# Kernel optimization log

Measured on AMD Instinct MI355X. Metric: run time of the kernel, lower is better.

Reference implementation:

```python
import jax, jax.numpy as jnp
import numpy as np

V, E, H, R, RD = 32000, 300, 300, 50, 50  # vocab, word-emb, hidden, rel vocab, rel emb
B, N = 32, 128                            # trees per batch, nodes per tree


def setup_inputs() -> dict:
    key = jax.random.key(0)
    ks = jax.random.split(key, 10)
    root_hidden = jax.random.normal(ks[0], (B, H), jnp.float32)
    relations = jax.random.randint(ks[1], (B, N), 0, R, jnp.int32)
    prev_words = jax.random.randint(ks[2], (B, N), 0, V, jnp.int32)
    # topologically sorted parent pointers: parent[i] in [-1, i-1]; -1 = virtual root
    rng = np.random.default_rng(0)
    parents = np.full((B, N), -1, dtype=np.int32)
    for i in range(1, N):
        parents[:, i] = rng.integers(-1, i, size=B)
    parents = jnp.asarray(parents)
    s_in = 1.0 / np.float32(np.sqrt(RD + E))
    s_h = 1.0 / np.float32(np.sqrt(H))
    emb = jax.random.normal(ks[3], (V, E), jnp.float32) * 0.02
    rel_emb = jax.random.normal(ks[4], (R, RD), jnp.float32) * 0.02
    W_ih = jax.random.normal(ks[5], (4 * H, RD + E), jnp.float32) * s_in
    W_hh = jax.random.normal(ks[6], (4 * H, H), jnp.float32) * s_h
    b_ih = jnp.zeros((4 * H,), jnp.float32)
    b_hh = jnp.zeros((4 * H,), jnp.float32)
    W_out = jax.random.normal(ks[7], (V, H), jnp.float32) * s_h
    b_out = jnp.zeros((V,), jnp.float32)
    return {"root_hidden": root_hidden, "relations": relations, "prev_words": prev_words,
            "parents": parents, "emb": emb, "rel_emb": rel_emb, "W_ih": W_ih, "W_hh": W_hh,
            "b_ih": b_ih, "b_hh": b_hh, "W_out": W_out, "b_out": b_out}


def reference(root_hidden, relations, prev_words, parents, emb, rel_emb,
              W_ih, W_hh, b_ih, b_hh, W_out, b_out):
    # per-node input: rel embedding ++ (teacher-forced) previous word embedding
    x = jnp.concatenate([rel_emb[relations], emb[prev_words]], axis=-1)  # [B,N,RD+E]
    xg = jnp.einsum('bni,gi->bng', x, W_ih) + b_ih                       # [B,N,4H]

    def one_tree(h0, xg_t, pars):
        n = pars.shape[0]
        h_buf = jnp.zeros((n + 1, H), xg_t.dtype).at[0].set(h0)
        c_buf = jnp.zeros((n + 1, H), xg_t.dtype).at[0].set(h0)  # original: hidden=(h,h)

        def step(carry, inp):
            hb, cb = carry
            xg_i, par, idx = inp
            ph = hb[par + 1]
            pc = cb[par + 1]
            gates = xg_i + ph @ W_hh.T + b_hh
            i_g, f_g, g_g, o_g = jnp.split(gates, 4)
            c = jax.nn.sigmoid(f_g) * pc + jax.nn.sigmoid(i_g) * jnp.tanh(g_g)
            h = jax.nn.sigmoid(o_g) * jnp.tanh(c)
            return (hb.at[idx + 1].set(h), cb.at[idx + 1].set(c)), h

        _, hs = jax.lax.scan(step, (h_buf, c_buf), (xg_t, pars, jnp.arange(n)))
        return hs  # [N,H]

    hs = jax.vmap(one_tree)(root_hidden, xg, parents)          # [B,N,H]
    logits = jnp.einsum('bnh,vh->bnv', hs, W_out) + b_out      # [B,N,V]
    return logits
```

## Files before the change

kernel.cpp:

```cpp
#include <hip/hip_runtime.h>
#include <hip/hip_bf16.h>

typedef unsigned short u16;
typedef unsigned int u32;
typedef unsigned long long u64;
typedef __attribute__((ext_vector_type(8))) short short8;
typedef __attribute__((ext_vector_type(4))) float f32x4;

#define NB 32
#define NN 128
#define HH 300
#define NV 32000
#define KP 320
#define KX 352
#define XGS 1280

#define NSLICE 15
#define UPS 20
#define NROWS 80
#define TPBS 320
#define GMAXN 16
#define LDW 328

#define A_LD(p)     __hip_atomic_load((p), __ATOMIC_RELAXED, __HIP_MEMORY_SCOPE_AGENT)
#define A_ST(p, v)  __hip_atomic_store((p), (v), __ATOMIC_RELAXED, __HIP_MEMORY_SCOPE_AGENT)
#define A_ADD(p, v) __hip_atomic_fetch_add((p), (v), __ATOMIC_RELAXED, __HIP_MEMORY_SCOPE_AGENT)

__device__ __forceinline__ float sigm(float x) { return 1.f / (1.f + __expf(-x)); }
__device__ __forceinline__ float tanh_f(float x) {
    float e = __expf(2.f * x);
    return 1.f - 2.f / (e + 1.f);
}
__device__ __forceinline__ u16 f2bf(float f) {
    __hip_bfloat16 b = __float2bfloat16(f);
    return *reinterpret_cast<u16*>(&b);
}

__global__ void k_init(const float* __restrict__ rh, u16* __restrict__ hb16,
                       int* __restrict__ lvl_done) {
    const int stride = gridDim.x * blockDim.x;
    const int idx = blockIdx.x * blockDim.x + threadIdx.x;
    for (int e = idx; e < NB * 129 * 20; e += stride) {
        int row = e / 20, c = 300 + (e - row * 20);
        hb16[(size_t)row * KP + c] = 0;
    }
    for (int e = idx; e < NB * HH; e += stride) {
        int b = e / HH, u = e - b * HH;
        hb16[(size_t)(b * 129) * KP + u] = f2bf(rh[e]);
    }
    for (int e = idx; e < NB * NN; e += stride) lvl_done[e] = 0;
}

__global__ void k_pack(const float* __restrict__ W_ih, const float* __restrict__ W_hh,
                       u16* __restrict__ Wihp, u16* __restrict__ Wp16) {
    const int tot = 1280 * KX + NSLICE * NROWS * LDW;
    for (int n = blockIdx.x * blockDim.x + threadIdx.x; n < tot; n += gridDim.x * blockDim.x) {
        if (n < 1280 * KX) {
            int r = n / KX, k = n - r * KX;
            float v = (r < 1200 && k < 350) ? W_ih[r * 350 + k] : 0.f;
            Wihp[n] = f2bf(v);
        } else {
            int m = n - 1280 * KX;
            int s = m / (NROWS * LDW);
            int rem = m - s * (NROWS * LDW);
            int r = rem / LDW, k = rem - r * LDW;
            int g = r / UPS, ul = r - g * UPS;
            int grow = g * HH + s * UPS + ul;
            float v = (k < HH) ? W_hh[grow * HH + k] : 0.f;
            Wp16[m] = f2bf(v);
        }
    }
}

__global__ void k_gatherX(const int* __restrict__ relations, const int* __restrict__ prev_words,
                          const float* __restrict__ rel_emb, const float* __restrict__ emb,
                          u16* __restrict__ X) {
    for (int e = blockIdx.x * blockDim.x + threadIdx.x; e < NB * NN * KX;
         e += gridDim.x * blockDim.x) {
        int node = e / KX, c = e - node * KX;
        float v = 0.f;
        if (c < 50) v = rel_emb[relations[node] * 50 + c];
        else if (c < 350) v = emb[(size_t)prev_words[node] * 300 + (c - 50)];
        X[e] = f2bf(v);
    }
}

__global__ void k_prep(const int* __restrict__ parents, int* __restrict__ lvl_nodes,
                       int* __restrict__ lvl_cnt, int* __restrict__ lvl_start,
                       int* __restrict__ nlev) {
    __shared__ int dep[NB][NN];
    __shared__ int cnt[NB][NN];
    __shared__ int st[NB][NN];
    const int t = threadIdx.x;
    if (t < NB) {
        for (int l = 0; l < NN; ++l) cnt[t][l] = 0;
        int md = 0;
        for (int i = 0; i < NN; ++i) {
            int p = parents[t * NN + i];
            int d = (p < 0) ? 0 : dep[t][p] + 1;
            dep[t][i] = d;
            cnt[t][d]++;
            md = max(md, d);
        }
        nlev[t] = md + 1;
        int run = 0;
        for (int l = 0; l < NN; ++l) {
            st[t][l] = run;
            lvl_start[t * NN + l] = run;
            lvl_cnt[t * NN + l] = cnt[t][l];
            run += cnt[t][l];
        }
        for (int i = 0; i < NN; ++i) {
            int d = dep[t][i];
            lvl_nodes[t * NN + st[t][d]] = i;
            st[t][d]++;
        }
    }
}

__global__ __launch_bounds__(256) void k_xgemm(const u16* __restrict__ Xbf,
                                               const u16* __restrict__ Wihp,
                                               const float* __restrict__ b_ih,
                                               float* __restrict__ xg) {
    __shared__ __align__(16) u16 As[128 * 40];
    __shared__ __align__(16) u16 Bs[128 * 40];
    const int tid = threadIdx.x;
    const int lane = tid & 63, wv = tid >> 6;
    const int wm = wv >> 1, wn = wv & 1;
    const int mblk = blockIdx.x, nblk = blockIdx.y;
    const u16* Ag = Xbf + (size_t)mblk * 128 * KX;
    const u16* Bg = Wihp + (size_t)nblk * 128 * KX;
    f32x4 acc[4][4] = {};
    const int lrow = lane & 15, lseg = lane >> 4;
    for (int kk = 0; kk < KX; kk += 32) {
#pragma unroll
        for (int q = 0; q < 2; ++q) {
            int s = tid + q * 256;
            int r = s >> 2, seg = s & 3;
            *(uint4*)&As[r * 40 + seg * 8] = *(const uint4*)&Ag[(size_t)r * KX + kk + seg * 8];
            *(uint4*)&Bs[r * 40 + seg * 8] = *(const uint4*)&Bg[(size_t)r * KX + kk + seg * 8];
        }
        __syncthreads();
        short8 av[4], bv[4];
#pragma unroll
        for (int i = 0; i < 4; ++i) {
            av[i] = *(const short8*)&As[(wm * 64 + i * 16 + lrow) * 40 + lseg * 8];
            bv[i] = *(const short8*)&Bs[(wn * 64 + i * 16 + lrow) * 40 + lseg * 8];
        }
#pragma unroll
        for (int i = 0; i < 4; ++i)
#pragma unroll
            for (int j = 0; j < 4; ++j)
                acc[i][j] = __builtin_amdgcn_mfma_f32_16x16x32_bf16(bv[j], av[i], acc[i][j],
                                                                    0, 0, 0);
        __syncthreads();
    }
#pragma unroll
    for (int i = 0; i < 4; ++i) {
        const int row = mblk * 128 + wm * 64 + i * 16 + lrow;
        float* orow = xg + (size_t)row * XGS;
#pragma unroll
        for (int j = 0; j < 4; ++j) {
            const int col = nblk * 128 + wn * 64 + j * 16 + lseg * 4;
            f32x4 v = acc[i][j];
            if (col < 1200) {
                f32x4 bo = *(const f32x4*)&b_ih[col];
                v[0] += bo[0]; v[1] += bo[1]; v[2] += bo[2]; v[3] += bo[3];
            }
            *(f32x4*)&orow[col] = v;
        }
    }
}

__global__ __launch_bounds__(TPBS) void k_scan(const int* __restrict__ parents,
                                               const u16* __restrict__ Wp16,
                                               const float* __restrict__ xg,
                                               const float* __restrict__ b_hh,
                                               const float* __restrict__ rh,
                                               u16* __restrict__ hb16,
                                               const int* __restrict__ lvl_nodes,
                                               const int* __restrict__ lvl_cnt,
                                               const int* __restrict__ lvl_start,
                                               const int* __restrict__ nlev,
                                               int* __restrict__ lvl_done) {
    __shared__ __align__(16) u16 Wl[NROWS * LDW];
    __shared__ __align__(16) u16 hs[GMAXN * LDW];
    __shared__ __align__(16) float gates[GMAXN * 82];
    __shared__ float c_lds[129 * UPS];
    __shared__ int nid_s[GMAXN], par_s[GMAXN];

    const int t = threadIdx.x;
    const int b = blockIdx.x / NSLICE;
    const int s = blockIdx.x % NSLICE;
    const int lane = t & 63, wv = t >> 6;
    const int lrow = lane & 15, lk = lane >> 4;

    {
        const u64* src = (const u64*)(Wp16 + (size_t)s * NROWS * LDW);
        u64* dst = (u64*)Wl;
        for (int e = t; e < NROWS * LDW / 4; e += TPBS) dst[e] = src[e];
    }
    if (t < UPS) c_lds[t] = rh[b * HH + s * UPS + t];
    __syncthreads();

    const int nl = nlev[b];
    for (int l = 0; l < nl; ++l) {
        const int cnt = lvl_cnt[b * NN + l];
        const int start = lvl_start[b * NN + l];
        for (int off = 0; off < cnt; off += GMAXN) {
            const int gc = min(GMAXN, cnt - off);
            if (t < gc) {
                int i = lvl_nodes[b * NN + start + off + t];
                nid_s[t] = i;
                par_s[t] = parents[b * NN + i];
            }
            __syncthreads();
            for (int e = t; e < gc * 80; e += TPBS) {
                const int j = e / 80, q = e - j * 80;
                const u64* hrow = (const u64*)(hb16 +
                    (size_t)(b * 129 + par_s[j] + 1) * KP);
                *(u64*)&hs[j * LDW + q * 4] = A_LD(&hrow[q]);
            }
            __syncthreads();
            {
                f32x4 acc = {};
#pragma unroll
                for (int kk = 0; kk < KP; kk += 32) {
                    short8 av = *(const short8*)&hs[lrow * LDW + kk + lk * 8];
                    short8 bv = *(const short8*)&Wl[(wv * 16 + lrow) * LDW + kk + lk * 8];
                    acc = __builtin_amdgcn_mfma_f32_16x16x32_bf16(av, bv, acc, 0, 0, 0);
                }
#pragma unroll
                for (int r = 0; r < 4; ++r)
                    gates[(lk * 4 + r) * 82 + wv * 16 + lrow] = acc[r];
            }
            __syncthreads();
            if (t < 160) {
                const int j = t / 10, up = t - j * 10;
                if (j < gc) {
                    const int i = nid_s[j];
                    const int par = par_s[j];
                    const int ul0 = up * 2;
                    const float* gj = gates + j * 82;
                    const float* xgp = xg + (size_t)(b * NN + i) * XGS + s * UPS;
                    const float* bhp = b_hh + s * UPS;
                    float hv[2];
#pragma unroll
                    for (int un = 0; un < 2; ++un) {
                        const int ul = ul0 + un;
                        float gs[4];
#pragma unroll
                        for (int g = 0; g < 4; ++g)
                            gs[g] = gj[g * UPS + ul] + xgp[g * HH + ul] + bhp[g * HH + ul];
                        const float pc = c_lds[(par + 1) * UPS + ul];
                        const float cv = sigm(gs[1]) * pc + sigm(gs[0]) * tanh_f(gs[2]);
                        hv[un] = sigm(gs[3]) * tanh_f(cv);
                        c_lds[(i + 1) * UPS + ul] = cv;
                    }
                    const u32 hp = (u32)f2bf(hv[0]) | ((u32)f2bf(hv[1]) << 16);
                    A_ST((u32*)(hb16 + (size_t)(b * 129 + i + 1) * KP + s * UPS + ul0), hp);
                }
            }
            __syncthreads();
        }
        if (l + 1 < nl) {
            if (t == 0) {
                int* dp = &lvl_done[b * NN + l];
                const int old = A_ADD(dp, 1);
                if (old != NSLICE - 1) {
                    while (A_LD(dp) < NSLICE) __builtin_amdgcn_s_sleep(1);
                }
            }
            __syncthreads();
        }
    }
}

__global__ void k_cast_B(const float* __restrict__ W_out, u16* __restrict__ Bm) {
    for (int e = blockIdx.x * blockDim.x + threadIdx.x; e < NV * KP;
         e += gridDim.x * blockDim.x) {
        int v = e / KP, k = e - v * KP;
        float x = (k < HH) ? W_out[v * HH + k] : 0.f;
        Bm[e] = f2bf(x);
    }
}

__global__ __launch_bounds__(256) void k_gemm(const u16* __restrict__ hb16,
                                              const u16* __restrict__ Bbf,
                                              const float* __restrict__ b_out,
                                              float* __restrict__ out) {
    __shared__ __align__(16) u16 As[128 * 40];
    __shared__ __align__(16) u16 Bs[128 * 40];
    const int tid = threadIdx.x;
    const int lane = tid & 63, wv = tid >> 6;
    const int wm = wv >> 1, wn = wv & 1;
    const int bid = blockIdx.x;
    const int newbid = (bid & 7) * 1000 + (bid >> 3);
    const int mblk = newbid & 31, nblk = newbid >> 5;
    const u16* Ag = hb16 + ((size_t)mblk * 129 + 1) * KP;
    const u16* Bg = Bbf + (size_t)nblk * 128 * KP;
    f32x4 acc[4][4] = {};
    const int lrow = lane & 15, lseg = lane >> 4;
    for (int kk = 0; kk < KP; kk += 32) {
#pragma unroll
        for (int q = 0; q < 2; ++q) {
            int s = tid + q * 256;
            int r = s >> 2, seg = s & 3;
            *(uint4*)&As[r * 40 + seg * 8] = *(const uint4*)&Ag[r * KP + kk + seg * 8];
            *(uint4*)&Bs[r * 40 + seg * 8] = *(const uint4*)&Bg[r * KP + kk + seg * 8];
        }
        __syncthreads();
        short8 av[4], bv[4];
#pragma unroll
        for (int i = 0; i < 4; ++i) {
            av[i] = *(const short8*)&As[(wm * 64 + i * 16 + lrow) * 40 + lseg * 8];
            bv[i] = *(const short8*)&Bs[(wn * 64 + i * 16 + lrow) * 40 + lseg * 8];
        }
#pragma unroll
        for (int i = 0; i < 4; ++i)
#pragma unroll
            for (int j = 0; j < 4; ++j)
                acc[i][j] = __builtin_amdgcn_mfma_f32_16x16x32_bf16(bv[j], av[i], acc[i][j],
                                                                    0, 0, 0);
        __syncthreads();
    }
#pragma unroll
    for (int i = 0; i < 4; ++i) {
        const int row = mblk * 128 + wm * 64 + i * 16 + lrow;
        float* orow = out + (size_t)row * NV;
#pragma unroll
        for (int j = 0; j < 4; ++j) {
            const int col = nblk * 128 + wn * 64 + j * 16 + lseg * 4;
            f32x4 v = acc[i][j];
            f32x4 bo = *(const f32x4*)&b_out[col];
            v[0] += bo[0]; v[1] += bo[1]; v[2] += bo[2]; v[3] += bo[3];
            __builtin_nontemporal_store(v, (f32x4*)&orow[col]);
        }
    }
}

extern "C" void kernel_launch(void* const* d_in, const int* in_sizes, int n_in,
                              void* d_out, int out_size, void* d_ws, size_t ws_size,
                              hipStream_t stream) {
    const float* root_hidden = (const float*)d_in[0];
    const int* relations = (const int*)d_in[1];
    const int* prev_words = (const int*)d_in[2];
    const int* parents = (const int*)d_in[3];
    const float* emb = (const float*)d_in[4];
    const float* rel_emb = (const float*)d_in[5];
    const float* W_ih = (const float*)d_in[6];
    const float* W_hh = (const float*)d_in[7];
    const float* b_ih = (const float*)d_in[8];
    const float* b_hh = (const float*)d_in[9];
    const float* W_out = (const float*)d_in[10];
    const float* b_out = (const float*)d_in[11];
    float* out = (float*)d_out;

    float* xg = (float*)d_ws;
    u16* Xbf = (u16*)(xg + 4096 * XGS);
    u16* Wihp = Xbf + 4096 * KX;
    u16* Wp16 = Wihp + 1280 * KX;
    u16* hb16 = Wp16 + NSLICE * NROWS * LDW;
    u16* Bbf = hb16 + 1320960;
    int* lvl_nodes = (int*)(Bbf + 10240000);
    int* lvl_cnt = lvl_nodes + 4096;
    int* lvl_start = lvl_cnt + 4096;
    int* nlev = lvl_start + 4096;
    int* lvl_done = nlev + 64;

    k_init<<<128, 256, 0, stream>>>(root_hidden, hb16, lvl_done);
    k_pack<<<1024, 256, 0, stream>>>(W_ih, W_hh, Wihp, Wp16);
    k_gatherX<<<1024, 256, 0, stream>>>(relations, prev_words, rel_emb, emb, Xbf);
    k_prep<<<1, 64, 0, stream>>>(parents, lvl_nodes, lvl_cnt, lvl_start, nlev);

    k_xgemm<<<dim3(32, 10), 256, 0, stream>>>(Xbf, Wihp, b_ih, xg);

    k_scan<<<dim3(NB * NSLICE), dim3(TPBS), 0, stream>>>(
        parents, Wp16, xg, b_hh, root_hidden, hb16,
        lvl_nodes, lvl_cnt, lvl_start, nlev, lvl_done);

    k_cast_B<<<4096, 256, 0, stream>>>(W_out, Bbf);
    k_gemm<<<dim3(8000), 256, 0, stream>>>(hb16, Bbf, b_out, out);
}
```

Before: 341.7 us.

## Fuse tree scan, W_out cast and output GEMM into one persistent kernel

Merges the level-synchronous LSTM scan, the W_out bf16 cast and the logits GEMM into a single launch with block-role dispatch. GEMM blocks spin on per-tree completion and cast-completion counters, so output tiles for finished trees can start while other trees are still scanning. The GEMM tile widens to 128x256 with 512 threads. This removes launch gaps and serialization, but it relies on scan and cast blocks being scheduled before the spinning GEMM blocks, which risks stalls or deadlock. It also raises scan block size to 512 threads, of which 3 warps sit idle.

```diff
diff --git a/kernel.cpp b/kernel.cpp
--- a/kernel.cpp
+++ b/kernel.cpp
@@ -18,9 +18,21 @@
 #define NSLICE 15
 #define UPS 20
 #define NROWS 80
-#define TPBS 320
 #define GMAXN 16
 #define LDW 328
+
+#define TPB 512
+#define SCANB (NB * NSLICE)
+#define CASTB 128
+#define GEMMB (125 * 32)
+
+#define SM_WL 0
+#define SM_HS 52480
+#define SM_GATES 62976
+#define SM_CL 68224
+#define SM_NID 78544
+#define SM_PAR 78608
+#define SM_BYTES 78720
 
 #define A_LD(p)     __hip_atomic_load((p), __ATOMIC_RELAXED, __HIP_MEMORY_SCOPE_AGENT)
 #define A_ST(p, v)  __hip_atomic_store((p), (v), __ATOMIC_RELAXED, __HIP_MEMORY_SCOPE_AGENT)
@@ -37,7 +49,8 @@
 }
 
 __global__ void k_init(const float* __restrict__ rh, u16* __restrict__ hb16,
-                       int* __restrict__ lvl_done) {
+                       int* __restrict__ lvl_done, int* __restrict__ tree_done,
+                       int* __restrict__ cast_done) {
     const int stride = gridDim.x * blockDim.x;
     const int idx = blockIdx.x * blockDim.x + threadIdx.x;
     for (int e = idx; e < NB * 129 * 20; e += stride) {
@@ -49,6 +62,8 @@
         hb16[(size_t)(b * 129) * KP + u] = f2bf(rh[e]);
     }
     for (int e = idx; e < NB * NN; e += stride) lvl_done[e] = 0;
+    if (idx < NB) tree_done[idx] = 0;
+    if (idx == 0) cast_done[0] = 0;
 }
 
 __global__ void k_pack(const float* __restrict__ W_ih, const float* __restrict__ W_hh,
@@ -172,169 +187,193 @@
     }
 }
 
-__global__ __launch_bounds__(TPBS) void k_scan(const int* __restrict__ parents,
-                                               const u16* __restrict__ Wp16,
-                                               const float* __restrict__ xg,
-                                               const float* __restrict__ b_hh,
-                                               const float* __restrict__ rh,
-                                               u16* __restrict__ hb16,
-                                               const int* __restrict__ lvl_nodes,
-                                               const int* __restrict__ lvl_cnt,
-                                               const int* __restrict__ lvl_start,
-                                               const int* __restrict__ nlev,
-                                               int* __restrict__ lvl_done) {
-    __shared__ __align__(16) u16 Wl[NROWS * LDW];
-    __shared__ __align__(16) u16 hs[GMAXN * LDW];
-    __shared__ __align__(16) float gates[GMAXN * 82];
-    __shared__ float c_lds[129 * UPS];
-    __shared__ int nid_s[GMAXN], par_s[GMAXN];
-
+__global__ __launch_bounds__(TPB, 4) void k_fused(const int* __restrict__ parents,
+                                                  const u16* __restrict__ Wp16,
+                                                  const float* __restrict__ xg,
+                                                  const float* __restrict__ b_hh,
+                                                  const float* __restrict__ rh,
+                                                  u16* __restrict__ hb16,
+                                                  const int* __restrict__ lvl_nodes,
+                                                  const int* __restrict__ lvl_cnt,
+                                                  const int* __restrict__ lvl_start,
+                                                  const int* __restrict__ nlev,
+                                                  int* __restrict__ lvl_done,
+                                                  int* __restrict__ tree_done,
+                                                  const float* __restrict__ W_out,
+                                                  u16* __restrict__ Bbf,
+                                                  int* __restrict__ cast_done,
+                                                  const float* __restrict__ b_out,
+                                                  float* __restrict__ out) {
+    __shared__ __align__(16) char smem[SM_BYTES];
     const int t = threadIdx.x;
-    const int b = blockIdx.x / NSLICE;
-    const int s = blockIdx.x % NSLICE;
-    const int lane = t & 63, wv = t >> 6;
-    const int lrow = lane & 15, lk = lane >> 4;
-
-    {
-        const u64* src = (const u64*)(Wp16 + (size_t)s * NROWS * LDW);
-        u64* dst = (u64*)Wl;
-        for (int e = t; e < NROWS * LDW / 4; e += TPBS) dst[e] = src[e];
-    }
-    if (t < UPS) c_lds[t] = rh[b * HH + s * UPS + t];
-    __syncthreads();
-
-    const int nl = nlev[b];
-    for (int l = 0; l < nl; ++l) {
-        const int cnt = lvl_cnt[b * NN + l];
-        const int start = lvl_start[b * NN + l];
-        for (int off = 0; off < cnt; off += GMAXN) {
-            const int gc = min(GMAXN, cnt - off);
-            if (t < gc) {
-                int i = lvl_nodes[b * NN + start + off + t];
-                nid_s[t] = i;
-                par_s[t] = parents[b * NN + i];
+
+    if (blockIdx.x < SCANB) {
+        u16* Wl = (u16*)(smem + SM_WL);
+        u16* hs = (u16*)(smem + SM_HS);
+        float* gates = (float*)(smem + SM_GATES);
+        float* c_lds = (float*)(smem + SM_CL);
+        int* nid_s = (int*)(smem + SM_NID);
+        int* par_s = (int*)(smem + SM_PAR);
+
+        const int b = blockIdx.x / NSLICE;
+        const int s = blockIdx.x % NSLICE;
+        const int lane = t & 63, wv = t >> 6;
+        const int lrow = lane & 15, lk = lane >> 4;
+
+        {
+            const u64* src = (const u64*)(Wp16 + (size_t)s * NROWS * LDW);
+            u64* dst = (u64*)Wl;
+            for (int e = t; e < NROWS * LDW / 4; e += TPB) dst[e] = src[e];
+        }
+        if (t < UPS) c_lds[t] = rh[b * HH + s * UPS + t];
+        __syncthreads();
+
+        const int nl = nlev[b];
+        for (int l = 0; l < nl; ++l) {
+            const int cnt = lvl_cnt[b * NN + l];
+            const int start = lvl_start[b * NN + l];
+            for (int off = 0; off < cnt; off += GMAXN) {
+                const int gc = min(GMAXN, cnt - off);
+                if (t < gc) {
+                    int i = lvl_nodes[b * NN + start + off + t];
+                    nid_s[t] = i;
+                    par_s[t] = parents[b * NN + i];
+                }
+                __syncthreads();
+                for (int e = t; e < gc * 80; e += TPB) {
+                    const int j = e / 80, q = e - j * 80;
+                    const u64* hrow = (const u64*)(hb16 +
+                        (size_t)(b * 129 + par_s[j] + 1) * KP);
+                    *(u64*)&hs[j * LDW + q * 4] = A_LD(&hrow[q]);
+                }
+                __syncthreads();
+                if (wv < 5) {
+                    f32x4 acc = {};
+#pragma unroll
+                    for (int kk = 0; kk < KP; kk += 32) {
+                        short8 av = *(const short8*)&hs[lrow * LDW + kk + lk * 8];
+                        short8 bv = *(const short8*)&Wl[(wv * 16 + lrow) * LDW + kk + lk * 8];
+                        acc = __builtin_amdgcn_mfma_f32_16x16x32_bf16(av, bv, acc, 0, 0, 0);
+                    }
+#pragma unroll
+                    for (int r = 0; r < 4; ++r)
+                        gates[(lk * 4 + r) * 82 + wv * 16 + lrow] = acc[r];
+                }
+                __syncthreads();
+                if (t < 160) {
+                    const int j = t / 10, up = t - j * 10;
+                    if (j < gc) {
+                        const int i = nid_s[j];
+                        const int par = par_s[j];
+                        const int ul0 = up * 2;
+                        const float* gj = gates + j * 82;
+                        const float* xgp = xg + (size_t)(b * NN + i) * XGS + s * UPS;
+                        const float* bhp = b_hh + s * UPS;
+                        float hv[2];
+#pragma unroll
+                        for (int un = 0; un < 2; ++un) {
+                            const int ul = ul0 + un;
+                            float gs[4];
+#pragma unroll
+                            for (int g = 0; g < 4; ++g)
+                                gs[g] = gj[g * UPS + ul] + xgp[g * HH + ul] + bhp[g * HH + ul];
+                            const float pc = c_lds[(par + 1) * UPS + ul];
+                            const float cv = sigm(gs[1]) * pc + sigm(gs[0]) * tanh_f(gs[2]);
+                            hv[un] = sigm(gs[3]) * tanh_f(cv);
+                            c_lds[(i + 1) * UPS + ul] = cv;
+                        }
+                        const u32 hp = (u32)f2bf(hv[0]) | ((u32)f2bf(hv[1]) << 16);
+                        A_ST((u32*)(hb16 + (size_t)(b * 129 + i + 1) * KP + s * UPS + ul0), hp);
+                    }
+                }
+                __syncthreads();
+            }
+            if (l + 1 < nl) {
+                if (t == 0) {
+                    int* dp = &lvl_done[b * NN + l];
+                    const int old = A_ADD(dp, 1);
+                    if (old != NSLICE - 1) {
+                        while (A_LD(dp) < NSLICE) __builtin_amdgcn_s_sleep(1);
+                    }
+                }
+                __syncthreads();
+            }
+        }
+        if (t == 0) A_ADD(&tree_done[b], 1);
+    } else if (blockIdx.x < SCANB + CASTB) {
+        const int cb = blockIdx.x - SCANB;
+        const int per = NV * KP / 4 / CASTB;
+        u64* Bq = (u64*)Bbf;
+        for (int e = cb * per + t; e < (cb + 1) * per; e += TPB) {
+            const int c4 = e * 4;
+            const int v = c4 / KP, k = c4 - v * KP;
+            const float* wr = W_out + (size_t)v * HH;
+            float x0 = 0.f, x1 = 0.f, x2 = 0.f, x3 = 0.f;
+            if (k + 0 < HH) x0 = wr[k + 0];
+            if (k + 1 < HH) x1 = wr[k + 1];
+            if (k + 2 < HH) x2 = wr[k + 2];
+            if (k + 3 < HH) x3 = wr[k + 3];
+            u64 pk = (u64)f2bf(x0) | ((u64)f2bf(x1) << 16) |
+                     ((u64)f2bf(x2) << 32) | ((u64)f2bf(x3) << 48);
+            A_ST(&Bq[e], pk);
+        }
+        __syncthreads();
+        if (t == 0) A_ADD(cast_done, 1);
+    } else {
+        u16* As = (u16*)smem;
+        u16* Bs = (u16*)(smem + 10240);
+        const int gid = blockIdx.x - SCANB - CASTB;
+        const int nblk = gid / NB;
+        const int mblk = gid % NB;
+        if (t == 0) {
+            while (A_LD(&tree_done[mblk]) < NSLICE || A_LD(cast_done) < CASTB)
+                __builtin_amdgcn_s_sleep(16);
+        }
+        __syncthreads();
+        const int lane = t & 63, wv = t >> 6;
+        const int wm = wv >> 2, wn = wv & 3;
+        const int lrow = lane & 15, lseg = lane >> 4;
+        const u16* Ag = hb16 + ((size_t)mblk * 129 + 1) * KP;
+        const u16* Bg = Bbf + (size_t)nblk * 256 * KP;
+        f32x4 acc[4][4] = {};
+        for (int kk = 0; kk < KP; kk += 32) {
+            {
+                int r = t >> 2, seg = t & 3;
+                *(uint4*)&As[r * 40 + seg * 8] = *(const uint4*)&Ag[(size_t)r * KP + kk + seg * 8];
+            }
+#pragma unroll
+            for (int q = 0; q < 2; ++q) {
+                int sI = t + q * 512;
+                int r = sI >> 2, seg = sI & 3;
+                *(uint4*)&Bs[r * 40 + seg * 8] = *(const uint4*)&Bg[(size_t)r * KP + kk + seg * 8];
             }
             __syncthreads();
-            for (int e = t; e < gc * 80; e += TPBS) {
-                const int j = e / 80, q = e - j * 80;
-                const u64* hrow = (const u64*)(hb16 +
-                    (size_t)(b * 129 + par_s[j] + 1) * KP);
-                *(u64*)&hs[j * LDW + q * 4] = A_LD(&hrow[q]);
-            }
+            short8 av[4], bv[4];
+#pragma unroll
+            for (int i = 0; i < 4; ++i) {
+                av[i] = *(const short8*)&As[(wm * 64 + i * 16 + lrow) * 40 + lseg * 8];
+                bv[i] = *(const short8*)&Bs[(wn * 64 + i * 16 + lrow) * 40 + lseg * 8];
+            }
+#pragma unroll
+            for (int i = 0; i < 4; ++i)
+#pragma unroll
+                for (int j = 0; j < 4; ++j)
+                    acc[i][j] = __builtin_amdgcn_mfma_f32_16x16x32_bf16(bv[j], av[i], acc[i][j],
+                                                                        0, 0, 0);
             __syncthreads();
-            {
-                f32x4 acc = {};
-#pragma unroll
-                for (int kk = 0; kk < KP; kk += 32) {
-                    short8 av = *(const short8*)&hs[lrow * LDW + kk + lk * 8];
-                    short8 bv = *(const short8*)&Wl[(wv * 16 + lrow) * LDW + kk + lk * 8];
-                    acc = __builtin_amdgcn_mfma_f32_16x16x32_bf16(av, bv, acc, 0, 0, 0);
-                }
-#pragma unroll
-                for (int r = 0; r < 4; ++r)
-                    gates[(lk * 4 + r) * 82 + wv * 16 + lrow] = acc[r];
-            }
-            __syncthreads();
-            if (t < 160) {
-                const int j = t / 10, up = t - j * 10;
-                if (j < gc) {
-                    const int i = nid_s[j];
-                    const int par = par_s[j];
-                    const int ul0 = up * 2;
-                    const float* gj = gates + j * 82;
-                    const float* xgp = xg + (size_t)(b * NN + i) * XGS + s * UPS;
-                    const float* bhp = b_hh + s * UPS;
-                    float hv[2];
-#pragma unroll
-                    for (int un = 0; un < 2; ++un) {
-                        const int ul = ul0 + un;
-                        float gs[4];
-#pragma unroll
-                        for (int g = 0; g < 4; ++g)
-                            gs[g] = gj[g * UPS + ul] + xgp[g * HH + ul] + bhp[g * HH + ul];
-                        const float pc = c_lds[(par + 1) * UPS + ul];
-                        const float cv = sigm(gs[1]) * pc + sigm(gs[0]) * tanh_f(gs[2]);
-                        hv[un] = sigm(gs[3]) * tanh_f(cv);
-                        c_lds[(i + 1) * UPS + ul] = cv;
-                    }
-                    const u32 hp = (u32)f2bf(hv[0]) | ((u32)f2bf(hv[1]) << 16);
-                    A_ST((u32*)(hb16 + (size_t)(b * 129 + i + 1) * KP + s * UPS + ul0), hp);
-                }
-            }
-            __syncthreads();
-        }
-        if (l + 1 < nl) {
-            if (t == 0) {
-                int* dp = &lvl_done[b * NN + l];
-                const int old = A_ADD(dp, 1);
-                if (old != NSLICE - 1) {
-                    while (A_LD(dp) < NSLICE) __builtin_amdgcn_s_sleep(1);
-                }
-            }
-            __syncthreads();
-        }
-    }
-}
-
-__global__ void k_cast_B(const float* __restrict__ W_out, u16* __restrict__ Bm) {
-    for (int e = blockIdx.x * blockDim.x + threadIdx.x; e < NV * KP;
-         e += gridDim.x * blockDim.x) {
-        int v = e / KP, k = e - v * KP;
-        float x = (k < HH) ? W_out[v * HH + k] : 0.f;
-        Bm[e] = f2bf(x);
-    }
-}
-
-__global__ __launch_bounds__(256) void k_gemm(const u16* __restrict__ hb16,
-                                              const u16* __restrict__ Bbf,
-                                              const float* __restrict__ b_out,
-                                              float* __restrict__ out) {
-    __shared__ __align__(16) u16 As[128 * 40];
-    __shared__ __align__(16) u16 Bs[128 * 40];
-    const int tid = threadIdx.x;
-    const int lane = tid & 63, wv = tid >> 6;
-    const int wm = wv >> 1, wn = wv & 1;
-    const int bid = blockIdx.x;
-    const int newbid = (bid & 7) * 1000 + (bid >> 3);
-    const int mblk = newbid & 31, nblk = newbid >> 5;
-    const u16* Ag = hb16 + ((size_t)mblk * 129 + 1) * KP;
-    const u16* Bg = Bbf + (size_t)nblk * 128 * KP;
-    f32x4 acc[4][4] = {};
-    const int lrow = lane & 15, lseg = lane >> 4;
-    for (int kk = 0; kk < KP; kk += 32) {
-#pragma unroll
-        for (int q = 0; q < 2; ++q) {
-            int s = tid + q * 256;
-            int r = s >> 2, seg = s & 3;
-            *(uint4*)&As[r * 40 + seg * 8] = *(const uint4*)&Ag[r * KP + kk + seg * 8];
-            *(uint4*)&Bs[r * 40 + seg * 8] = *(const uint4*)&Bg[r * KP + kk + seg * 8];
-        }
-        __syncthreads();
-        short8 av[4], bv[4];
+        }
 #pragma unroll
         for (int i = 0; i < 4; ++i) {
-            av[i] = *(const short8*)&As[(wm * 64 + i * 16 + lrow) * 40 + lseg * 8];
-            bv[i] = *(const short8*)&Bs[(wn * 64 + i * 16 + lrow) * 40 + lseg * 8];
-        }
-#pragma unroll
-        for (int i = 0; i < 4; ++i)
-#pragma unroll
-            for (int j = 0; j < 4; ++j)
-                acc[i][j] = __builtin_amdgcn_mfma_f32_16x16x32_bf16(bv[j], av[i], acc[i][j],
-                                                                    0, 0, 0);
-        __syncthreads();
-    }
-#pragma unroll
-    for (int i = 0; i < 4; ++i) {
-        const int row = mblk * 128 + wm * 64 + i * 16 + lrow;
-        float* orow = out + (size_t)row * NV;
-#pragma unroll
-        for (int j = 0; j < 4; ++j) {
-            const int col = nblk * 128 + wn * 64 + j * 16 + lseg * 4;
-            f32x4 v = acc[i][j];
-            f32x4 bo = *(const f32x4*)&b_out[col];
-            v[0] += bo[0]; v[1] += bo[1]; v[2] += bo[2]; v[3] += bo[3];
-            __builtin_nontemporal_store(v, (f32x4*)&orow[col]);
+            const int row = mblk * 128 + wm * 64 + i * 16 + lrow;
+            float* orow = out + (size_t)row * NV;
+#pragma unroll
+            for (int j = 0; j < 4; ++j) {
+                const int col = nblk * 256 + wn * 64 + j * 16 + lseg * 4;
+                f32x4 v = acc[i][j];
+                f32x4 bo = *(const f32x4*)&b_out[col];
+                v[0] += bo[0]; v[1] += bo[1]; v[2] += bo[2]; v[3] += bo[3];
+                __builtin_nontemporal_store(v, (f32x4*)&orow[col]);
+            }
         }
     }
 }
@@ -367,18 +406,18 @@
     int* lvl_start = lvl_cnt + 4096;
     int* nlev = lvl_start + 4096;
     int* lvl_done = nlev + 64;
-
-    k_init<<<128, 256, 0, stream>>>(root_hidden, hb16, lvl_done);
+    int* tree_done = lvl_done + 4096;
+    int* cast_done = tree_done + 32;
+
+    k_init<<<128, 256, 0, stream>>>(root_hidden, hb16, lvl_done, tree_done, cast_done);
     k_pack<<<1024, 256, 0, stream>>>(W_ih, W_hh, Wihp, Wp16);
     k_gatherX<<<1024, 256, 0, stream>>>(relations, prev_words, rel_emb, emb, Xbf);
     k_prep<<<1, 64, 0, stream>>>(parents, lvl_nodes, lvl_cnt, lvl_start, nlev);
 
     k_xgemm<<<dim3(32, 10), 256, 0, stream>>>(Xbf, Wihp, b_ih, xg);
 
-    k_scan<<<dim3(NB * NSLICE), dim3(TPBS), 0, stream>>>(
+    k_fused<<<dim3(SCANB + CASTB + GEMMB), dim3(TPB), 0, stream>>>(
         parents, Wp16, xg, b_hh, root_hidden, hb16,
-        lvl_nodes, lvl_cnt, lvl_start, nlev, lvl_done);
-
-    k_cast_B<<<4096, 256, 0, stream>>>(W_out, Bbf);
-    k_gemm<<<dim3(8000), 256, 0, stream>>>(hb16, Bbf, b_out, out);
-}
+        lvl_nodes, lvl_cnt, lvl_start, nlev, lvl_done, tree_done,
+        W_out, Bbf, cast_done, b_out, out);
+}
```

Result: slower. 358.7 us (+5.0%).
